# Optimization experiments

Hardware: AMD Instinct MI355X
Metric: run time of the kernel (lower is better)

## Reference

```python
import jax, jax.numpy as jnp
import numpy as np
from jax import lax

C = 384        # in_channels
K = 16         # number of frames selected (self.k)
SIGMA = 0.05   # perturbation sigma (forward arg, hardcoded)
NUM_SAMPLES = 500


def setup_inputs() -> dict:
    key = jax.random.key(0)
    ks = jax.random.split(key, 8)
    B, T, N = 16, 32, 196
    D = 2 * C  # PredictorLG embed_dim for 'tpool'
    w = lambda k, s: jax.random.normal(k, s, jnp.float32) * 0.02
    return {
        "x": jax.random.normal(ks[0], (B, T * N, C), jnp.float32),
        "noise": jax.random.normal(ks[1], (B, NUM_SAMPLES, T), jnp.float32),
        "ln_g": jnp.ones((D,), jnp.float32),
        "ln_b": jnp.zeros((D,), jnp.float32),
        "w_in": w(ks[2], (D, D)), "b_in": jnp.zeros((D,), jnp.float32),
        "w1": w(ks[3], (D, D // 2)), "b1": jnp.zeros((D // 2,), jnp.float32),
        "w2": w(ks[4], (D // 2, D // 4)), "b2": jnp.zeros((D // 4,), jnp.float32),
        "w3": w(ks[5], (D // 4, 1)), "b3": jnp.zeros((1,), jnp.float32),
        "N": N, "T": T,
    }


def _predictor(x_, ln_g, ln_b, w_in, b_in, w1, b1, w2, b2, w3, b3):
    # PredictorLG: LayerNorm -> Linear -> GELU -> local/global split -> MLP -> scalar score
    mu = x_.mean(-1, keepdims=True)
    var = x_.var(-1, keepdims=True)  # biased, matches nn.LayerNorm
    h = (x_ - mu) / jnp.sqrt(var + 1e-5) * ln_g + ln_b
    h = jax.nn.gelu(h @ w_in + b_in, approximate=False)
    half = h.shape[-1] // 2
    g = h[..., half:].mean(axis=1, keepdims=True)                      # global pool over T
    h = jnp.concatenate([h[..., :half], jnp.broadcast_to(g, h[..., :half].shape)], -1)
    h = jax.nn.gelu(h @ w1 + b1, approximate=False)
    h = jax.nn.gelu(h @ w2 + b2, approximate=False)
    return (h @ w3 + b3)[..., 0]                                       # (B, T)


def reference(x, noise, ln_g, ln_b, w_in, b_in, w1, b1, w2, b2, w3, b3, N, T):
    B = x.shape[0]
    xt = x.reshape(B, T, N, C)                                         # b t n c
    x_ = jnp.concatenate([xt.mean(2), xt.max(2)], -1)                  # (B, T, 2C)
    scores = _predictor(x_, ln_g, ln_b, w_in, b_in, w1, b1, w2, b2, w3, b3)
    lo = scores.min(-1, keepdims=True)
    hi = scores.max(-1, keepdims=True)
    scores = (scores - lo) / (hi - lo + 1e-5)                          # min_max_norm
    # PerturbedTopKFunction.forward
    perturbed = scores[:, None, :] + noise * SIGMA                     # (B, ns, T)
    idx = jnp.sort(lax.top_k(perturbed, K)[1], axis=-1)                # (B, ns, K)
    indicators = jax.nn.one_hot(idx, T, dtype=x.dtype).mean(1)         # (B, K, T)
    # extract_patches_from_indicators: einsum over flattened frames
    patches = jnp.einsum('bkt,btc->bkc', indicators, xt.reshape(B, T, N * C))
    return patches.reshape(B, K * N, C)                                # 'b k (n c) -> b (k n) c'
```

## Files before the change

kernel.cpp:

```cpp
#include <hip/hip_runtime.h>
#include <math.h>

#define CC 384
#define DD 768
#define TT 32
#define NN 196
#define BB 16
#define KK 16
#define NSAMP 500
#define JV 18816
#define FRAME 75264

__device__ __forceinline__ float gelu_exact(float x) {
    return 0.5f * x * (1.0f + erff(x * 0.70710678118654752440f));
}

__global__ __launch_bounds__(384) void pool_kernel(const float* __restrict__ x,
                                                   const float* __restrict__ ln_g,
                                                   const float* __restrict__ ln_b,
                                                   float* __restrict__ xbar) {
    int row = blockIdx.x;
    const float4* xp = (const float4*)(x + (size_t)row * NN * CC);
    int tx = threadIdx.x;
    int ty = threadIdx.y;
    float4 s = make_float4(0.f, 0.f, 0.f, 0.f);
    float4 m = make_float4(-INFINITY, -INFINITY, -INFINITY, -INFINITY);
    for (int n = ty; n < NN; n += 4) {
        float4 v = xp[n * 96 + tx];
        s.x += v.x; s.y += v.y; s.z += v.z; s.w += v.w;
        m.x = fmaxf(m.x, v.x); m.y = fmaxf(m.y, v.y);
        m.z = fmaxf(m.z, v.z); m.w = fmaxf(m.w, v.w);
    }
    __shared__ float4 ssum[4][96];
    __shared__ float4 smax[4][96];
    __shared__ float xf[DD];
    ssum[ty][tx] = s;
    smax[ty][tx] = m;
    __syncthreads();
    if (ty == 0) {
        for (int r = 1; r < 4; ++r) {
            float4 a = ssum[r][tx];
            s.x += a.x; s.y += a.y; s.z += a.z; s.w += a.w;
            float4 b = smax[r][tx];
            m.x = fmaxf(m.x, b.x); m.y = fmaxf(m.y, b.y);
            m.z = fmaxf(m.z, b.z); m.w = fmaxf(m.w, b.w);
        }
        const float invn = 1.0f / (float)NN;
        xf[4*tx+0] = s.x * invn; xf[4*tx+1] = s.y * invn;
        xf[4*tx+2] = s.z * invn; xf[4*tx+3] = s.w * invn;
        xf[CC + 4*tx+0] = m.x; xf[CC + 4*tx+1] = m.y;
        xf[CC + 4*tx+2] = m.z; xf[CC + 4*tx+3] = m.w;
    }
    __syncthreads();
    int tid = ty * 96 + tx;
    float e0 = xf[tid], e1 = xf[tid + CC];
    float ps = e0 + e1, pq = e0 * e0 + e1 * e1;
    #pragma unroll
    for (int off = 32; off; off >>= 1) {
        ps += __shfl_down(ps, off);
        pq += __shfl_down(pq, off);
    }
    __shared__ float red[12];
    __shared__ float mv[2];
    int wv = tid >> 6;
    if ((tid & 63) == 0) { red[wv] = ps; red[6 + wv] = pq; }
    __syncthreads();
    if (tid == 0) {
        float su = 0.f, sq = 0.f;
        #pragma unroll
        for (int i = 0; i < 6; ++i) { su += red[i]; sq += red[6 + i]; }
        float mean = su * (1.0f / DD);
        float var  = sq * (1.0f / DD) - mean * mean;
        mv[0] = mean;
        mv[1] = rsqrtf(var + 1e-5f);
    }
    __syncthreads();
    float mean = mv[0], inv = mv[1];
    float* o = xbar + (size_t)row * DD;
    o[tid]      = (e0 - mean) * inv * ln_g[tid]      + ln_b[tid];
    o[tid + CC] = (e1 - mean) * inv * ln_g[tid + CC] + ln_b[tid + CC];
}

__global__ __launch_bounds__(1024) void fcin_kernel(const float* __restrict__ xbar,
                                                    const float* __restrict__ w_in,
                                                    const float* __restrict__ b_in,
                                                    float* __restrict__ h1) {
    __shared__ float xs[4][DD];
    __shared__ float pacc[4][4][256];
    int tid = threadIdx.x;
    int row0 = blockIdx.x * 4;
    int col0 = blockIdx.y * 256;

    if (tid < 768) {
        int r = tid / 192, j = tid % 192;
        ((float4*)xs[r])[j] = *(const float4*)(xbar + (size_t)(row0 + r) * DD + 4 * j);
    }
    __syncthreads();

    int kg = tid >> 8;
    int c  = tid & 255;
    int col = col0 + c;
    int k0 = kg * 192;
    float a0 = 0.f, a1 = 0.f, a2 = 0.f, a3 = 0.f;
    const float* wp = w_in + (size_t)k0 * DD + col;
    #pragma unroll 4
    for (int i = 0; i < 192; ++i) {
        float wv = wp[(size_t)i * DD];
        a0 += xs[0][k0 + i] * wv;
        a1 += xs[1][k0 + i] * wv;
        a2 += xs[2][k0 + i] * wv;
        a3 += xs[3][k0 + i] * wv;
    }
    pacc[kg][0][c] = a0; pacc[kg][1][c] = a1;
    pacc[kg][2][c] = a2; pacc[kg][3][c] = a3;
    __syncthreads();

    int rr = tid >> 8;
    float s = b_in[col] + pacc[0][rr][c] + pacc[1][rr][c]
                        + pacc[2][rr][c] + pacc[3][rr][c];
    h1[(size_t)(row0 + rr) * DD + col] = gelu_exact(s);
}

__global__ __launch_bounds__(128) void gpoolG_kernel(const float* __restrict__ h1,
                                                     const float* __restrict__ w1,
                                                     float* __restrict__ G) {
    __shared__ float gs[CC];
    int tid = threadIdx.x;
    int b = blockIdx.x;
    const float* hb = h1 + (size_t)b * TT * DD + CC;
    for (int i = tid; i < CC; i += 128) {
        float s = 0.f;
        #pragma unroll 8
        for (int t = 0; t < TT; ++t) s += hb[(size_t)t * DD + i];
        gs[i] = s * (1.0f / TT);
    }
    __syncthreads();
    int col = blockIdx.y * 128 + tid;
    float acc = 0.f;
    const float* wp = w1 + (size_t)CC * CC + col;
    #pragma unroll 8
    for (int i = 0; i < CC; ++i)
        acc += gs[i] * wp[(size_t)i * CC];
    G[b * CC + col] = acc;
}

__global__ __launch_bounds__(768) void mlp1_kernel(const float* __restrict__ h1,
                                                   const float* __restrict__ G,
                                                   const float* __restrict__ w1,
                                                   const float* __restrict__ b1,
                                                   float* __restrict__ h2) {
    __shared__ float xs[4][CC];
    __shared__ float pacc[4][4][192];
    int tid = threadIdx.x;
    int row0 = blockIdx.x * 4;
    int col0 = blockIdx.y * 192;
    int b = row0 >> 5;

    if (tid < 384) {
        int r = tid / 96, j = tid % 96;
        ((float4*)xs[r])[j] = *(const float4*)(h1 + (size_t)(row0 + r) * DD + 4 * j);
    }
    __syncthreads();

    int kg = tid / 192;
    int c  = tid % 192;
    int col = col0 + c;
    int k0 = kg * 96;
    float a0 = 0.f, a1 = 0.f, a2 = 0.f, a3 = 0.f;
    const float* wp = w1 + (size_t)k0 * CC + col;
    #pragma unroll 4
    for (int i = 0; i < 96; ++i) {
        float wv = wp[(size_t)i * CC];
        a0 += xs[0][k0 + i] * wv;
        a1 += xs[1][k0 + i] * wv;
        a2 += xs[2][k0 + i] * wv;
        a3 += xs[3][k0 + i] * wv;
    }
    pacc[kg][0][c] = a0; pacc[kg][1][c] = a1;
    pacc[kg][2][c] = a2; pacc[kg][3][c] = a3;
    __syncthreads();

    int rr = tid / 192;
    float s = b1[col] + G[b * CC + col]
            + pacc[0][rr][c] + pacc[1][rr][c] + pacc[2][rr][c] + pacc[3][rr][c];
    h2[(size_t)(row0 + rr) * CC + col] = gelu_exact(s);
}

__global__ __launch_bounds__(192) void score_kernel(const float* __restrict__ h2,
                                                    const float* __restrict__ w2,
                                                    const float* __restrict__ b2,
                                                    const float* __restrict__ w3,
                                                    float* __restrict__ scores) {
    __shared__ float h2row[CC];
    int row = blockIdx.x, tid = threadIdx.x;

    if (tid < 96)
        ((float4*)h2row)[tid] = ((const float4*)(h2 + (size_t)row * CC))[tid];
    __syncthreads();

    float a = b2[tid];
    const float* wp = w2 + tid;
    #pragma unroll 8
    for (int k = 0; k < CC; ++k)
        a += h2row[k] * wp[(size_t)k * 192];
    float v = gelu_exact(a) * w3[tid];
    #pragma unroll
    for (int off = 32; off; off >>= 1) v += __shfl_down(v, off);
    __shared__ float red[3];
    if ((tid & 63) == 0) red[tid >> 6] = v;
    __syncthreads();
    if (tid == 0) scores[row] = red[0] + red[1] + red[2];
}

__global__ __launch_bounds__(512) void topk_kernel(const float* __restrict__ scores,
                                                   const float* __restrict__ noise,
                                                   float* __restrict__ ind) {
    __shared__ float ns[TT];
    __shared__ float mnmx[2];
    __shared__ int counts[KK * TT];
    int b = blockIdx.x, tid = threadIdx.x;

    if (tid < TT) ns[tid] = scores[b * TT + tid];
    counts[tid] = 0;
    __syncthreads();
    if (tid == 0) {
        float mn = ns[0], mx = ns[0];
        for (int t = 1; t < TT; ++t) { mn = fminf(mn, ns[t]); mx = fmaxf(mx, ns[t]); }
        mnmx[0] = mn; mnmx[1] = mx;
    }
    __syncthreads();
    if (tid < TT) ns[tid] = (ns[tid] - mnmx[0]) / (mnmx[1] - mnmx[0] + 1e-5f);
    __syncthreads();

    if (tid < NSAMP) {
        const float* nb = noise + ((size_t)b * NSAMP + tid) * TT;
        float p[TT];
        #pragma unroll
        for (int t = 0; t < TT; ++t) p[t] = ns[t] + nb[t] * 0.05f;
        int k = 0;
        #pragma unroll
        for (int t = 0; t < TT; ++t) {
            int rank = 0;
            #pragma unroll
            for (int u = 0; u < TT; ++u)
                rank += (p[u] > p[t] || (p[u] == p[t] && u < t)) ? 1 : 0;
            if (rank < KK) { atomicAdd(&counts[k * TT + t], 1); ++k; }
        }
    }
    __syncthreads();
    ind[b * (KK * TT) + tid] = (float)counts[tid] * (1.0f / NSAMP);
}

__global__ __launch_bounds__(256) void gather_kernel(const float* __restrict__ x,
                                                     const float* __restrict__ ind,
                                                     float* __restrict__ out) {
    __shared__ float w[KK * TT];
    __shared__ int act[TT];
    __shared__ int nact_s;
    int b = blockIdx.y;
    int tid = threadIdx.x;
    w[tid] = ind[b * (KK * TT) + tid];
    w[256 + tid] = ind[b * (KK * TT) + 256 + tid];
    __syncthreads();
    if (tid < TT) {
        float s = 0.f;
        #pragma unroll
        for (int k = 0; k < KK; ++k) s += w[k * TT + tid];
        unsigned long long m = __ballot(s != 0.f);
        if (s != 0.f) act[__popcll(m & ((1ull << tid) - 1ull))] = tid;
        if (tid == 0) nact_s = (int)__popcll(m);
    }
    __syncthreads();
    int nact = nact_s;

    int j4 = blockIdx.x * 256 + tid;
    if (j4 >= JV) return;

    const float4* xb = (const float4*)(x + (size_t)b * TT * FRAME);
    float4 acc[KK];
    #pragma unroll
    for (int k = 0; k < KK; ++k) acc[k] = make_float4(0.f, 0.f, 0.f, 0.f);

    for (int it = 0; it < nact; ++it) {
        int t = act[it];
        float4 v = xb[(size_t)t * JV + j4];
        #pragma unroll
        for (int k = 0; k < KK; ++k) {
            float wk = w[k * TT + t];
            acc[k].x += wk * v.x; acc[k].y += wk * v.y;
            acc[k].z += wk * v.z; acc[k].w += wk * v.w;
        }
    }
    float4* ob = (float4*)(out + (size_t)b * KK * FRAME);
    #pragma unroll
    for (int k = 0; k < KK; ++k)
        ob[(size_t)k * JV + j4] = acc[k];
}

extern "C" void kernel_launch(void* const* d_in, const int* in_sizes, int n_in,
                              void* d_out, int out_size, void* d_ws, size_t ws_size,
                              hipStream_t stream) {
    const float* x     = (const float*)d_in[0];
    const float* noise = (const float*)d_in[1];
    const float* ln_g  = (const float*)d_in[2];
    const float* ln_b  = (const float*)d_in[3];
    const float* w_in  = (const float*)d_in[4];
    const float* b_in  = (const float*)d_in[5];
    const float* w1    = (const float*)d_in[6];
    const float* b1    = (const float*)d_in[7];
    const float* w2    = (const float*)d_in[8];
    const float* b2    = (const float*)d_in[9];
    const float* w3    = (const float*)d_in[10];
    const float* b3    = (const float*)d_in[11];
    (void)b3;
    float* out = (float*)d_out;

    float* ws     = (float*)d_ws;
    float* xbar   = ws;
    float* h1     = xbar + 512 * DD;
    float* h2     = h1 + 512 * DD;
    float* G      = h2 + 512 * CC;
    float* scores = G + BB * CC;
    float* ind    = scores + 512;

    hipLaunchKernelGGL(pool_kernel, dim3(BB * TT), dim3(96, 4), 0, stream,
                       x, ln_g, ln_b, xbar);
    hipLaunchKernelGGL(fcin_kernel, dim3(128, 3), dim3(1024), 0, stream,
                       xbar, w_in, b_in, h1);
    hipLaunchKernelGGL(gpoolG_kernel, dim3(BB, 3), dim3(128), 0, stream,
                       h1, w1, G);
    hipLaunchKernelGGL(mlp1_kernel, dim3(128, 2), dim3(768), 0, stream,
                       h1, G, w1, b1, h2);
    hipLaunchKernelGGL(score_kernel, dim3(512), dim3(192), 0, stream,
                       h2, w2, b2, w3, scores);
    hipLaunchKernelGGL(topk_kernel, dim3(BB), dim3(512), 0, stream,
                       scores, noise, ind);
    hipLaunchKernelGGL(gather_kernel, dim3((JV + 255) / 256, BB), dim3(256), 0, stream,
                       x, ind, out);
}
```

Before: 140.0 us.

## Fold global-pool projection into fcin and mlp1, drop gpoolG kernel

Removes the separate gpoolG kernel. fcin now writes per-4-row partial sums of the global half of h1. mlp1 reduces the 8 partials per batch into shared memory and computes the global-branch matmul alongside the local one. Both inner GEMV loops are also restructured to read four k-steps at a time with float4 shared loads. This saves one launch and a pass over h1, but every mlp1 block now redundantly recomputes the global projection for its batch, adding weight reads.

After: 120.4 us, median of 2. 14.0% less time.

```diff
diff --git a/kernel.cpp b/kernel.cpp
--- a/kernel.cpp
+++ b/kernel.cpp
@@ -84,11 +84,13 @@
 __global__ __launch_bounds__(1024) void fcin_kernel(const float* __restrict__ xbar,
                                                     const float* __restrict__ w_in,
                                                     const float* __restrict__ b_in,
-                                                    float* __restrict__ h1) {
+                                                    float* __restrict__ h1,
+                                                    float* __restrict__ Gpart) {
     __shared__ float xs[4][DD];
     __shared__ float pacc[4][4][256];
     int tid = threadIdx.x;
-    int row0 = blockIdx.x * 4;
+    int rowg = blockIdx.x;
+    int row0 = rowg * 4;
     int col0 = blockIdx.y * 256;
 
     if (tid < 768) {
@@ -103,13 +105,20 @@
     int k0 = kg * 192;
     float a0 = 0.f, a1 = 0.f, a2 = 0.f, a3 = 0.f;
     const float* wp = w_in + (size_t)k0 * DD + col;
-    #pragma unroll 4
-    for (int i = 0; i < 192; ++i) {
-        float wv = wp[(size_t)i * DD];
-        a0 += xs[0][k0 + i] * wv;
-        a1 += xs[1][k0 + i] * wv;
-        a2 += xs[2][k0 + i] * wv;
-        a3 += xs[3][k0 + i] * wv;
+    #pragma unroll 2
+    for (int i = 0; i < 192; i += 4) {
+        float w0 = wp[(size_t)(i + 0) * DD];
+        float w1v = wp[(size_t)(i + 1) * DD];
+        float w2v = wp[(size_t)(i + 2) * DD];
+        float w3v = wp[(size_t)(i + 3) * DD];
+        float4 x0 = *(const float4*)&xs[0][k0 + i];
+        float4 x1 = *(const float4*)&xs[1][k0 + i];
+        float4 x2 = *(const float4*)&xs[2][k0 + i];
+        float4 x3 = *(const float4*)&xs[3][k0 + i];
+        a0 += x0.x * w0 + x0.y * w1v + x0.z * w2v + x0.w * w3v;
+        a1 += x1.x * w0 + x1.y * w1v + x1.z * w2v + x1.w * w3v;
+        a2 += x2.x * w0 + x2.y * w1v + x2.z * w2v + x2.w * w3v;
+        a3 += x3.x * w0 + x3.y * w1v + x3.z * w2v + x3.w * w3v;
     }
     pacc[kg][0][c] = a0; pacc[kg][1][c] = a1;
     pacc[kg][2][c] = a2; pacc[kg][3][c] = a3;
@@ -118,46 +127,40 @@
     int rr = tid >> 8;
     float s = b_in[col] + pacc[0][rr][c] + pacc[1][rr][c]
                         + pacc[2][rr][c] + pacc[3][rr][c];
-    h1[(size_t)(row0 + rr) * DD + col] = gelu_exact(s);
-}
-
-__global__ __launch_bounds__(128) void gpoolG_kernel(const float* __restrict__ h1,
-                                                     const float* __restrict__ w1,
-                                                     float* __restrict__ G) {
-    __shared__ float gs[CC];
-    int tid = threadIdx.x;
-    int b = blockIdx.x;
-    const float* hb = h1 + (size_t)b * TT * DD + CC;
-    for (int i = tid; i < CC; i += 128) {
-        float s = 0.f;
-        #pragma unroll 8
-        for (int t = 0; t < TT; ++t) s += hb[(size_t)t * DD + i];
-        gs[i] = s * (1.0f / TT);
-    }
-    __syncthreads();
-    int col = blockIdx.y * 128 + tid;
-    float acc = 0.f;
-    const float* wp = w1 + (size_t)CC * CC + col;
-    #pragma unroll 8
-    for (int i = 0; i < CC; ++i)
-        acc += gs[i] * wp[(size_t)i * CC];
-    G[b * CC + col] = acc;
+    float g = gelu_exact(s);
+    h1[(size_t)(row0 + rr) * DD + col] = g;
+    pacc[0][rr][c] = g;
+    __syncthreads();
+
+    if (rr == 0 && col >= CC) {
+        float gsum = pacc[0][0][c] + pacc[0][1][c] + pacc[0][2][c] + pacc[0][3][c];
+        Gpart[(size_t)rowg * CC + (col - CC)] = gsum;
+    }
 }
 
 __global__ __launch_bounds__(768) void mlp1_kernel(const float* __restrict__ h1,
-                                                   const float* __restrict__ G,
+                                                   const float* __restrict__ Gpart,
                                                    const float* __restrict__ w1,
                                                    const float* __restrict__ b1,
                                                    float* __restrict__ h2) {
     __shared__ float xs[4][CC];
-    __shared__ float pacc[4][4][192];
+    __shared__ float gs[CC];
+    __shared__ float pacc[4][5][192];
     int tid = threadIdx.x;
-    int row0 = blockIdx.x * 4;
+    int rowg = blockIdx.x;
+    int row0 = rowg * 4;
+    int b = row0 >> 5;
     int col0 = blockIdx.y * 192;
-    int b = row0 >> 5;
-
-    if (tid < 384) {
-        int r = tid / 96, j = tid % 96;
+
+    if (tid < CC) {
+        float s = 0.f;
+        const float* gp = Gpart + (size_t)(b * 8) * CC + tid;
+        #pragma unroll
+        for (int rg = 0; rg < 8; ++rg) s += gp[(size_t)rg * CC];
+        gs[tid] = s * (1.0f / 32.0f);
+    } else {
+        int e = tid - CC;
+        int r = e / 96, j = e % 96;
         ((float4*)xs[r])[j] = *(const float4*)(h1 + (size_t)(row0 + r) * DD + 4 * j);
     }
     __syncthreads();
@@ -166,23 +169,40 @@
     int c  = tid % 192;
     int col = col0 + c;
     int k0 = kg * 96;
-    float a0 = 0.f, a1 = 0.f, a2 = 0.f, a3 = 0.f;
-    const float* wp = w1 + (size_t)k0 * CC + col;
-    #pragma unroll 4
-    for (int i = 0; i < 96; ++i) {
-        float wv = wp[(size_t)i * CC];
-        a0 += xs[0][k0 + i] * wv;
-        a1 += xs[1][k0 + i] * wv;
-        a2 += xs[2][k0 + i] * wv;
-        a3 += xs[3][k0 + i] * wv;
+    float a0 = 0.f, a1 = 0.f, a2 = 0.f, a3 = 0.f, ag = 0.f;
+    const float* wl = w1 + (size_t)k0 * CC + col;
+    const float* wg = w1 + (size_t)(CC + k0) * CC + col;
+    #pragma unroll 2
+    for (int i = 0; i < 96; i += 4) {
+        float l0 = wl[(size_t)(i + 0) * CC];
+        float l1 = wl[(size_t)(i + 1) * CC];
+        float l2 = wl[(size_t)(i + 2) * CC];
+        float l3 = wl[(size_t)(i + 3) * CC];
+        float g0 = wg[(size_t)(i + 0) * CC];
+        float g1 = wg[(size_t)(i + 1) * CC];
+        float g2 = wg[(size_t)(i + 2) * CC];
+        float g3 = wg[(size_t)(i + 3) * CC];
+        float4 x0 = *(const float4*)&xs[0][k0 + i];
+        float4 x1 = *(const float4*)&xs[1][k0 + i];
+        float4 x2 = *(const float4*)&xs[2][k0 + i];
+        float4 x3 = *(const float4*)&xs[3][k0 + i];
+        float4 gv = *(const float4*)&gs[k0 + i];
+        a0 += x0.x * l0 + x0.y * l1 + x0.z * l2 + x0.w * l3;
+        a1 += x1.x * l0 + x1.y * l1 + x1.z * l2 + x1.w * l3;
+        a2 += x2.x * l0 + x2.y * l1 + x2.z * l2 + x2.w * l3;
+        a3 += x3.x * l0 + x3.y * l1 + x3.z * l2 + x3.w * l3;
+        ag += gv.x * g0 + gv.y * g1 + gv.z * g2 + gv.w * g3;
     }
     pacc[kg][0][c] = a0; pacc[kg][1][c] = a1;
     pacc[kg][2][c] = a2; pacc[kg][3][c] = a3;
+    pacc[kg][4][c] = ag;
     __syncthreads();
 
     int rr = tid / 192;
-    float s = b1[col] + G[b * CC + col]
-            + pacc[0][rr][c] + pacc[1][rr][c] + pacc[2][rr][c] + pacc[3][rr][c];
+    float s = b1[col];
+    #pragma unroll
+    for (int kk = 0; kk < 4; ++kk)
+        s += pacc[kk][rr][c] + pacc[kk][4][c];
     h2[(size_t)(row0 + rr) * CC + col] = gelu_exact(s);
 }
 
@@ -318,19 +338,17 @@
     float* ws     = (float*)d_ws;
     float* xbar   = ws;
     float* h1     = xbar + 512 * DD;
-    float* h2     = h1 + 512 * DD;
-    float* G      = h2 + 512 * CC;
-    float* scores = G + BB * CC;
+    float* Gpart  = h1 + 512 * DD;
+    float* h2     = Gpart + 128 * CC;
+    float* scores = h2 + 512 * CC;
     float* ind    = scores + 512;
 
     hipLaunchKernelGGL(pool_kernel, dim3(BB * TT), dim3(96, 4), 0, stream,
                        x, ln_g, ln_b, xbar);
     hipLaunchKernelGGL(fcin_kernel, dim3(128, 3), dim3(1024), 0, stream,
-                       xbar, w_in, b_in, h1);
-    hipLaunchKernelGGL(gpoolG_kernel, dim3(BB, 3), dim3(128), 0, stream,
-                       h1, w1, G);
+                       xbar, w_in, b_in, h1, Gpart);
     hipLaunchKernelGGL(mlp1_kernel, dim3(128, 2), dim3(768), 0, stream,
-                       h1, G, w1, b1, h2);
+                       h1, Gpart, w1, b1, h2);
     hipLaunchKernelGGL(score_kernel, dim3(512), dim3(192), 0, stream,
                        h2, w2, b2, w3, scores);
     hipLaunchKernelGGL(topk_kernel, dim3(BB), dim3(512), 0, stream,
```
